# Kernel optimization log

Measured on AMD Instinct MI355X. Metric: run time of the kernel, lower is better.

The kernel has to match this reference:

```python
import jax, jax.numpy as jnp
import numpy as np

NUM_CLASSES = 80
ALPHA, GAMMA, BETA = 0.25, 2.0, 0.11
POS_THR, NEG_THR = 0.5, 0.4
B, A, G = 8, 98304, 32


def setup_inputs() -> dict:
    key = jax.random.key(0)
    k1, k2, k3, k4, k5, k6, k7 = jax.random.split(key, 7)
    # anchors: random centers/sizes over an ~800px image, xyxy format
    ctr = jax.random.uniform(k1, (A, 2), minval=50.0, maxval=750.0)
    wh = jax.random.uniform(k2, (A, 2), minval=16.0, maxval=256.0)
    anchors = jnp.concatenate([ctr - wh / 2, ctr + wh / 2], axis=-1)
    # gt boxes = jittered anchors so that positive (IoU>=0.5) matches exist
    idx = jax.random.randint(k3, (B, G), 0, A)
    gt_boxes = anchors[idx] + jax.random.normal(k4, (B, G, 4)) * 2.0
    gt_boxes = jnp.concatenate([
        jnp.minimum(gt_boxes[..., :2], gt_boxes[..., 2:] - 1.0),
        jnp.maximum(gt_boxes[..., 2:], gt_boxes[..., :2] + 1.0)], axis=-1)
    gt_labels = jax.random.randint(k5, (B, G), 1, NUM_CLASSES + 1)  # 1-indexed fg
    cls_predictions = jax.random.normal(k6, (B, A, NUM_CLASSES), dtype=jnp.float32)
    reg_predictions = jax.random.normal(k7, (B, A, 4), dtype=jnp.float32)
    return {"cls_predictions": cls_predictions, "reg_predictions": reg_predictions,
            "anchors": anchors, "gt_boxes": gt_boxes, "gt_labels": gt_labels}


def _pairwise_iou(boxes1, boxes2):  # [A,4],[G,4] -> [A,G]
    area1 = (boxes1[:, 2] - boxes1[:, 0]) * (boxes1[:, 3] - boxes1[:, 1])
    area2 = (boxes2[:, 2] - boxes2[:, 0]) * (boxes2[:, 3] - boxes2[:, 1])
    lt = jnp.maximum(boxes1[:, None, :2], boxes2[None, :, :2])
    rb = jnp.minimum(boxes1[:, None, 2:], boxes2[None, :, 2:])
    wh = jnp.clip(rb - lt, 0.0)
    inter = wh[..., 0] * wh[..., 1]
    return inter / (area1[:, None] + area2[None, :] - inter)


def _encode(matched, anchors):  # BoxCoder with weights (1,1,1,1)
    aw = anchors[:, 2] - anchors[:, 0]
    ah = anchors[:, 3] - anchors[:, 1]
    ax = anchors[:, 0] + 0.5 * aw
    ay = anchors[:, 1] + 0.5 * ah
    gw = matched[:, 2] - matched[:, 0]
    gh = matched[:, 3] - matched[:, 1]
    gx = matched[:, 0] + 0.5 * gw
    gy = matched[:, 1] + 0.5 * gh
    return jnp.stack([(gx - ax) / aw, (gy - ay) / ah,
                      jnp.log(gw / aw), jnp.log(gh / ah)], axis=-1)


def _match(anchors, gt_boxes_i, gt_labels_i):
    iou = _pairwise_iou(anchors, gt_boxes_i)          # [A, G]
    max_iou = iou.max(axis=-1)
    midx = iou.argmax(axis=-1)
    labels = gt_labels_i[midx]                        # [A]
    cls_t = jnp.where(max_iou >= POS_THR, labels,
                      jnp.where(max_iou < NEG_THR, 0, -1))
    reg_t = _encode(gt_boxes_i[midx], anchors)        # [A, 4]
    pos = max_iou >= POS_THR
    return cls_t, reg_t, pos


def reference(cls_predictions, reg_predictions, anchors, gt_boxes, gt_labels):
    cls_t, reg_t, pos = jax.vmap(_match, in_axes=(None, 0, 0))(anchors, gt_boxes, gt_labels)
    valid = (cls_t >= 0)[..., None].astype(cls_predictions.dtype)  # [B,A,1]
    fg = (cls_t > 0)[..., None].astype(cls_predictions.dtype)
    # one-hot targets (labels are 1-indexed; 0 = background -> all zeros)
    t = jax.nn.one_hot(cls_t - 1, NUM_CLASSES, dtype=cls_predictions.dtype) * fg
    x = cls_predictions
    bce = jnp.maximum(x, 0.0) - x * t + jnp.log1p(jnp.exp(-jnp.abs(x)))
    prob = jax.nn.sigmoid(x)
    p_t = prob * t + (1.0 - prob) * (1.0 - t)
    alpha_f = ALPHA * t + (1.0 - ALPHA) * (1.0 - t)
    focal = alpha_f * (1.0 - p_t) ** GAMMA * bce
    cls_sum = (focal * valid).sum()
    diff = jnp.abs(reg_predictions - reg_t)
    sl1 = jnp.where(diff < BETA, 0.5 * diff * diff / BETA, diff - 0.5 * BETA)
    posf = pos[..., None].astype(reg_predictions.dtype)
    reg_sum = (sl1 * posf).sum()
    num_pos = pos.sum().astype(cls_predictions.dtype)
    denom = jnp.maximum(num_pos, 1.0)
    cls_loss = jnp.where(num_pos > 0, cls_sum / denom, cls_sum)
    reg_loss = jnp.where(num_pos > 0, reg_sum / denom, 0.0)
    return (cls_loss + reg_loss, cls_loss, reg_loss)
```

## Files before the change

### kernel.cpp

```cpp
#include <hip/hip_runtime.h>
#include <math.h>

#define NUM_CLASSES 80
#define BETA 0.11f
#define POS_THR 0.5f
#define NEG_THR 0.4f
#define B_CNT 8
#define A_CNT 98304
#define G_CNT 32

#define FOCAL_BLOCKS 2048
#define FOCAL_STRIDE (FOCAL_BLOCKS * 256)
#define MATCH_BLOCKS ((B_CNT * A_CNT) / 256)

#define WS_FP   0
#define WS_MC   2048
#define WS_MR   (2048 + 3072)
#define WS_MP   (2048 + 2 * 3072)

__device__ __forceinline__ float focal0(float x) {
    const float e  = __expf(-fabsf(x));
    const float op = 1.0f + e;
    const float r  = __builtin_amdgcn_rcpf(op);
    const float prob = (x >= 0.0f) ? r : e * r;
    const float sp = fmaxf(x, 0.0f) + __logf(op);
    return 0.75f * prob * prob * sp;
}

__device__ __forceinline__ float focal1(float x) {
    const float e  = __expf(-fabsf(x));
    const float op = 1.0f + e;
    const float r  = __builtin_amdgcn_rcpf(op);
    const float prob = (x >= 0.0f) ? r : e * r;
    const float q  = 1.0f - prob;
    const float sp = fmaxf(-x, 0.0f) + __logf(op);
    return 0.25f * q * q * sp;
}

__device__ __forceinline__ float f0x4(float4 v) {
    return (focal0(v.x) + focal0(v.y)) + (focal0(v.z) + focal0(v.w));
}

__global__ __launch_bounds__(256) void focal_kernel(
    const float* __restrict__ cls_pred,
    float* __restrict__ ws)
{
    __shared__ float s_red[4];
    const int t = blockIdx.x * 256 + threadIdx.x;
    const float4* __restrict__ p = (const float4*)cls_pred;
    float sum = 0.0f;
    #pragma unroll
    for (int outer = 0; outer < 5; ++outer) {
        float4 v[6];
        #pragma unroll
        for (int j = 0; j < 6; ++j)
            v[j] = p[t + (outer * 6 + j) * FOCAL_STRIDE];
        #pragma unroll
        for (int j = 0; j < 6; ++j)
            sum += f0x4(v[j]);
    }
    #pragma unroll
    for (int off = 32; off > 0; off >>= 1) sum += __shfl_down(sum, off, 64);
    if ((threadIdx.x & 63) == 0) s_red[threadIdx.x >> 6] = sum;
    __syncthreads();
    if (threadIdx.x == 0)
        ws[WS_FP + blockIdx.x] = (s_red[0] + s_red[1]) + (s_red[2] + s_red[3]);
}

__global__ __launch_bounds__(256) void match_kernel(
    const float* __restrict__ cls_pred,
    const float* __restrict__ reg_pred,
    const float* __restrict__ anchors,
    const float* __restrict__ gt_boxes,
    const int*   __restrict__ gt_labels,
    float* __restrict__ ws)
{
    __shared__ float4 s_gt[G_CNT];
    __shared__ int    s_lab[G_CNT];
    __shared__ float  s_red[12];

    const int blocks_per_batch = A_CNT / 256;
    const int b = blockIdx.x / blocks_per_batch;
    const int a = (blockIdx.x % blocks_per_batch) * 256 + threadIdx.x;

    if (threadIdx.x < G_CNT) {
        s_gt[threadIdx.x]  = ((const float4*)gt_boxes)[b * G_CNT + threadIdx.x];
        s_lab[threadIdx.x] = gt_labels[b * G_CNT + threadIdx.x];
    }
    __syncthreads();

    const float4 an = ((const float4*)anchors)[a];
    const float aw = an.z - an.x;
    const float ah = an.w - an.y;
    const float area_a = aw * ah;

    float best = -1.0f;
    int bidx = 0;
    #pragma unroll
    for (int g = 0; g < G_CNT; ++g) {
        const float4 gb = s_gt[g];
        const float ltx = fmaxf(an.x, gb.x);
        const float lty = fmaxf(an.y, gb.y);
        const float rbx = fminf(an.z, gb.z);
        const float rby = fminf(an.w, gb.w);
        const float w = fmaxf(rbx - ltx, 0.0f);
        const float h = fmaxf(rby - lty, 0.0f);
        const float inter = w * h;
        const float area_g = (gb.z - gb.x) * (gb.w - gb.y);
        const float iou = inter / (area_a + area_g - inter);
        if (iou > best) { best = iou; bidx = g; }
    }

    const bool pos = (best >= POS_THR);
    const bool ign = (!pos) && (best >= NEG_THR);

    float regsum = 0.0f;
    float clsdelta = 0.0f;

    if (pos) {
        const float4 gb = s_gt[bidx];
        const float gw = gb.z - gb.x;
        const float gh = gb.w - gb.y;
        const float gx = gb.x + 0.5f * gw;
        const float gy = gb.y + 0.5f * gh;
        const float ax = an.x + 0.5f * aw;
        const float ay = an.y + 0.5f * ah;
        const float t0 = (gx - ax) / aw;
        const float t1 = (gy - ay) / ah;
        const float t2 = __logf(gw / aw);
        const float t3 = __logf(gh / ah);
        const float4 rp = ((const float4*)reg_pred)[b * A_CNT + a];
        const float d0 = fabsf(rp.x - t0);
        const float d1 = fabsf(rp.y - t1);
        const float d2 = fabsf(rp.z - t2);
        const float d3 = fabsf(rp.w - t3);
        const float s0 = (d0 < BETA) ? 0.5f * d0 * d0 / BETA : d0 - 0.5f * BETA;
        const float s1 = (d1 < BETA) ? 0.5f * d1 * d1 / BETA : d1 - 0.5f * BETA;
        const float s2 = (d2 < BETA) ? 0.5f * d2 * d2 / BETA : d2 - 0.5f * BETA;
        const float s3 = (d3 < BETA) ? 0.5f * d3 * d3 / BETA : d3 - 0.5f * BETA;
        regsum = (s0 + s1) + (s2 + s3);

        const int lab = s_lab[bidx];
        const float xt = cls_pred[(size_t)(b * A_CNT + a) * NUM_CLASSES + (lab - 1)];
        clsdelta = focal1(xt) - focal0(xt);
    } else if (ign) {
        const float4* __restrict__ row =
            (const float4*)(cls_pred + (size_t)(b * A_CNT + a) * NUM_CLASSES);
        float s = 0.0f;
        #pragma unroll
        for (int c = 0; c < NUM_CLASSES / 4; ++c) s += f0x4(row[c]);
        clsdelta = -s;
    }

    float v0 = clsdelta;
    float v1 = regsum;
    float v2 = pos ? 1.0f : 0.0f;
    #pragma unroll
    for (int off = 32; off > 0; off >>= 1) {
        v0 += __shfl_down(v0, off, 64);
        v1 += __shfl_down(v1, off, 64);
        v2 += __shfl_down(v2, off, 64);
    }
    const int wave = threadIdx.x >> 6;
    if ((threadIdx.x & 63) == 0) {
        s_red[wave] = v0; s_red[4 + wave] = v1; s_red[8 + wave] = v2;
    }
    __syncthreads();
    if (threadIdx.x == 0) {
        ws[WS_MC + blockIdx.x] = (s_red[0] + s_red[1]) + (s_red[2] + s_red[3]);
        ws[WS_MR + blockIdx.x] = (s_red[4] + s_red[5]) + (s_red[6] + s_red[7]);
        ws[WS_MP + blockIdx.x] = (s_red[8] + s_red[9]) + (s_red[10] + s_red[11]);
    }
}

__global__ __launch_bounds__(256) void finalize_kernel(
    const float* __restrict__ ws, float* __restrict__ out)
{
    __shared__ float s_red[12];
    float c = 0.0f, r = 0.0f, np = 0.0f;
    #pragma unroll
    for (int k = 0; k < FOCAL_BLOCKS / 256; ++k)
        c += ws[WS_FP + k * 256 + threadIdx.x];
    #pragma unroll
    for (int k = 0; k < MATCH_BLOCKS / 256; ++k) {
        c  += ws[WS_MC + k * 256 + threadIdx.x];
        r  += ws[WS_MR + k * 256 + threadIdx.x];
        np += ws[WS_MP + k * 256 + threadIdx.x];
    }
    #pragma unroll
    for (int off = 32; off > 0; off >>= 1) {
        c  += __shfl_down(c,  off, 64);
        r  += __shfl_down(r,  off, 64);
        np += __shfl_down(np, off, 64);
    }
    const int wave = threadIdx.x >> 6;
    if ((threadIdx.x & 63) == 0) {
        s_red[wave] = c; s_red[4 + wave] = r; s_red[8 + wave] = np;
    }
    __syncthreads();
    if (threadIdx.x == 0) {
        const float cs = (s_red[0] + s_red[1]) + (s_red[2] + s_red[3]);
        const float rs = (s_red[4] + s_red[5]) + (s_red[6] + s_red[7]);
        const float n  = (s_red[8] + s_red[9]) + (s_red[10] + s_red[11]);
        const float denom = fmaxf(n, 1.0f);
        const float cl = (n > 0.0f) ? cs / denom : cs;
        const float rl = (n > 0.0f) ? rs / denom : 0.0f;
        out[0] = cl + rl;
        out[1] = cl;
        out[2] = rl;
    }
}

extern "C" void kernel_launch(void* const* d_in, const int* in_sizes, int n_in,
                              void* d_out, int out_size, void* d_ws, size_t ws_size,
                              hipStream_t stream) {
    const float* cls_pred = (const float*)d_in[0];
    const float* reg_pred = (const float*)d_in[1];
    const float* anchors  = (const float*)d_in[2];
    const float* gt_boxes = (const float*)d_in[3];
    const int*   gt_labels= (const int*)d_in[4];
    float* out = (float*)d_out;
    float* ws  = (float*)d_ws;

    match_kernel<<<MATCH_BLOCKS, 256, 0, stream>>>(cls_pred, reg_pred, anchors,
                                                   gt_boxes, gt_labels, ws);
    focal_kernel<<<FOCAL_BLOCKS, 256, 0, stream>>>(cls_pred, ws);
    finalize_kernel<<<1, 256, 0, stream>>>(ws, out);
}
```

Baseline: 402.5 us.

## Fuse dense focal-loss sweep into the anchor matching kernel

Merges the separate focal-loss streaming kernel into the matching kernel. Each of the 3072 blocks now matches its anchors and also streams 20 float4s per thread of the class predictions, and one partial sum per block goes to the workspace. This removes a kernel launch and lets the IoU matching math overlap with memory streaming in the same waves. In exchange the fused blocks use more registers and the focal stride changes, which could hurt occupancy or memory coalescing balance.

New measurement: 371.2 us. -7.8%, faster.

```diff
diff --git a/kernel.cpp b/kernel.cpp
--- a/kernel.cpp
+++ b/kernel.cpp
@@ -9,14 +9,12 @@
 #define A_CNT 98304
 #define G_CNT 32
 
-#define FOCAL_BLOCKS 2048
-#define FOCAL_STRIDE (FOCAL_BLOCKS * 256)
-#define MATCH_BLOCKS ((B_CNT * A_CNT) / 256)
-
-#define WS_FP   0
-#define WS_MC   2048
-#define WS_MR   (2048 + 3072)
-#define WS_MP   (2048 + 2 * 3072)
+#define FUSED_BLOCKS ((B_CNT * A_CNT) / 256)
+#define FUSED_STRIDE (FUSED_BLOCKS * 256)
+
+#define WS_MC 0
+#define WS_MR FUSED_BLOCKS
+#define WS_MP (2 * FUSED_BLOCKS)
 
 __device__ __forceinline__ float focal0(float x) {
     const float e  = __expf(-fabsf(x));
@@ -41,33 +39,7 @@
     return (focal0(v.x) + focal0(v.y)) + (focal0(v.z) + focal0(v.w));
 }
 
-__global__ __launch_bounds__(256) void focal_kernel(
-    const float* __restrict__ cls_pred,
-    float* __restrict__ ws)
-{
-    __shared__ float s_red[4];
-    const int t = blockIdx.x * 256 + threadIdx.x;
-    const float4* __restrict__ p = (const float4*)cls_pred;
-    float sum = 0.0f;
-    #pragma unroll
-    for (int outer = 0; outer < 5; ++outer) {
-        float4 v[6];
-        #pragma unroll
-        for (int j = 0; j < 6; ++j)
-            v[j] = p[t + (outer * 6 + j) * FOCAL_STRIDE];
-        #pragma unroll
-        for (int j = 0; j < 6; ++j)
-            sum += f0x4(v[j]);
-    }
-    #pragma unroll
-    for (int off = 32; off > 0; off >>= 1) sum += __shfl_down(sum, off, 64);
-    if ((threadIdx.x & 63) == 0) s_red[threadIdx.x >> 6] = sum;
-    __syncthreads();
-    if (threadIdx.x == 0)
-        ws[WS_FP + blockIdx.x] = (s_red[0] + s_red[1]) + (s_red[2] + s_red[3]);
-}
-
-__global__ __launch_bounds__(256) void match_kernel(
+__global__ __launch_bounds__(256) void fused_kernel(
     const float* __restrict__ cls_pred,
     const float* __restrict__ reg_pred,
     const float* __restrict__ anchors,
@@ -152,7 +124,21 @@
         clsdelta = -s;
     }
 
-    float v0 = clsdelta;
+    const int t = blockIdx.x * 256 + threadIdx.x;
+    const float4* __restrict__ p = (const float4*)cls_pred;
+    float fsum = 0.0f;
+    #pragma unroll
+    for (int outer = 0; outer < 4; ++outer) {
+        float4 v[5];
+        #pragma unroll
+        for (int j = 0; j < 5; ++j)
+            v[j] = p[t + (outer * 5 + j) * FUSED_STRIDE];
+        #pragma unroll
+        for (int j = 0; j < 5; ++j)
+            fsum += f0x4(v[j]);
+    }
+
+    float v0 = clsdelta + fsum;
     float v1 = regsum;
     float v2 = pos ? 1.0f : 0.0f;
     #pragma unroll
@@ -179,10 +165,7 @@
     __shared__ float s_red[12];
     float c = 0.0f, r = 0.0f, np = 0.0f;
     #pragma unroll
-    for (int k = 0; k < FOCAL_BLOCKS / 256; ++k)
-        c += ws[WS_FP + k * 256 + threadIdx.x];
-    #pragma unroll
-    for (int k = 0; k < MATCH_BLOCKS / 256; ++k) {
+    for (int k = 0; k < FUSED_BLOCKS / 256; ++k) {
         c  += ws[WS_MC + k * 256 + threadIdx.x];
         r  += ws[WS_MR + k * 256 + threadIdx.x];
         np += ws[WS_MP + k * 256 + threadIdx.x];
@@ -222,8 +205,7 @@
     float* out = (float*)d_out;
     float* ws  = (float*)d_ws;
 
-    match_kernel<<<MATCH_BLOCKS, 256, 0, stream>>>(cls_pred, reg_pred, anchors,
+    fused_kernel<<<FUSED_BLOCKS, 256, 0, stream>>>(cls_pred, reg_pred, anchors,
                                                    gt_boxes, gt_labels, ws);
-    focal_kernel<<<FOCAL_BLOCKS, 256, 0, stream>>>(cls_pred, ws);
     finalize_kernel<<<1, 256, 0, stream>>>(ws, out);
 }
```
